# Performance work log

Measured on AMD Instinct MI355X. Metric: run time of the kernel, lower is better.

Reference implementation:

```python
import jax, jax.numpy as jnp
import numpy as np

N_HEAD = 16
HEAD_DIM = 64


def setup_inputs() -> dict:
    key = jax.random.key(0)
    k1, k2, k3 = jax.random.split(key, 3)
    B, T, C = 1, 4096, 1024
    x = jax.random.normal(k1, (B, T, C), dtype=jnp.float32)
    w_attn = jax.random.normal(k2, (3 * C, C), dtype=jnp.float32) * (C ** -0.5)
    w_proj = jax.random.normal(k3, (C, C), dtype=jnp.float32) * (C ** -0.5)
    return {"x": x, "w_attn": w_attn, "w_proj": w_proj}


def reference(x, w_attn, w_proj):
    B, T, C = x.shape
    H, D = N_HEAD, HEAD_DIM
    qkv = jnp.einsum('btc,fc->btf', x, w_attn)  # [B,T,3C]
    q, k, v = jnp.split(qkv, 3, axis=-1)
    # [B,H,T,D]
    q = q.reshape(B, T, H, D).transpose(0, 2, 1, 3)
    k = k.reshape(B, T, H, D).transpose(0, 2, 1, 3)
    v = v.reshape(B, T, H, D).transpose(0, 2, 1, 3)
    scale = 1.0 / (D ** 0.5)
    att = jnp.einsum('bhqd,bhkd->bhqk', q, k) * scale  # [B,H,T,T]
    causal = jnp.tril(jnp.ones((T, T), dtype=bool))
    att = jnp.where(causal[None, None], att, -jnp.inf)
    att = jax.nn.softmax(att, axis=-1)
    y = jnp.einsum('bhqk,bhkd->bhqd', att, v)  # [B,H,T,D]
    y = y.transpose(0, 2, 1, 3).reshape(B, T, C)
    return jnp.einsum('btc,oc->bto', y, w_proj)
```

## Files before the change

kernel.cpp:

```cpp
#include <hip/hip_runtime.h>

typedef unsigned short u16;
typedef __bf16 bf16x8 __attribute__((ext_vector_type(8)));
typedef float f32x4 __attribute__((ext_vector_type(4)));

__device__ __forceinline__ u16 f2bf(float f) {
  union { float f; unsigned u; } v; v.f = f;
  return (u16)((v.u + 0x7fffu + ((v.u >> 16) & 1u)) >> 16);
}
__device__ __forceinline__ float bf2f(u16 h) {
  union { unsigned u; float f; } v; v.u = ((unsigned)h) << 16;
  return v.f;
}

__device__ __forceinline__ unsigned pkbf(float lo, float hi) {
  union { float f; unsigned u; } a, b; a.f = lo; b.f = hi;
  return __builtin_amdgcn_perm(b.u + 0x8000u, a.u + 0x8000u, 0x07060302u);
}

__device__ __forceinline__ float fexp2(float x) {
#if __has_builtin(__builtin_amdgcn_exp2f)
  return __builtin_amdgcn_exp2f(x);
#else
  return exp2f(x);
#endif
}

__device__ __forceinline__ void gld16(const u16* g, u16* l) {
  __builtin_amdgcn_global_load_lds(
      (const __attribute__((address_space(1))) void*)g,
      (__attribute__((address_space(3))) void*)l, 16, 0, 0);
}


__global__ __launch_bounds__(256) void cvt3(
    const float* __restrict__ x, const float* __restrict__ wa,
    const float* __restrict__ wp, u16* __restrict__ xb,
    u16* __restrict__ wab, u16* __restrict__ wpb)
{
  int b = blockIdx.x;
  const float* in; u16* out; int i;
  if (b < 2048)      { in = x;  out = xb;  i = b * 256 + threadIdx.x; }
  else if (b < 3584) { in = wa; out = wab; i = (b - 2048) * 256 + threadIdx.x; }
  else               { in = wp; out = wpb; i = (b - 3584) * 256 + threadIdx.x; }
  const float* p = in + (size_t)i * 8;
  float4 a = *(const float4*)p, c = *(const float4*)(p + 4);
  uint4 o;
  o.x = pkbf(a.x, a.y); o.y = pkbf(a.z, a.w);
  o.z = pkbf(c.x, c.y); o.w = pkbf(c.z, c.w);
  *(uint4*)&out[(size_t)i * 8] = o;
}

__global__ __launch_bounds__(256) void combine2(
    const u16* __restrict__ O0, const u16* __restrict__ O1,
    const float* __restrict__ l0, const float* __restrict__ l1,
    u16* __restrict__ y)
{
  int i = blockIdx.x * 256 + threadIdx.x;
  int e0 = i * 8;
  int row = e0 >> 10, h = (e0 & 1023) >> 6;
  float inv = 1.0f / (l0[row * 16 + h] + l1[row * 16 + h]);
  uint4 a = *(const uint4*)&O0[(size_t)e0];
  uint4 b = *(const uint4*)&O1[(size_t)e0];
  unsigned aw[4] = {a.x, a.y, a.z, a.w}, bw[4] = {b.x, b.y, b.z, b.w};
  uint4 o;
  unsigned ow[4];
#pragma unroll
  for (int j = 0; j < 4; ++j) {
    float lo = (bf2f((u16)(aw[j] & 0xffffu)) + bf2f((u16)(bw[j] & 0xffffu))) * inv;
    float hi = (bf2f((u16)(aw[j] >> 16))     + bf2f((u16)(bw[j] >> 16)))     * inv;
    ow[j] = pkbf(lo, hi);
  }
  o.x = ow[0]; o.y = ow[1]; o.z = ow[2]; o.w = ow[3];
  *(uint4*)&y[(size_t)e0] = o;
}

template<bool COUT_F32, bool VSPLIT>
__global__ __launch_bounds__(256, 3) void gemm_lds(
    const u16* __restrict__ A, const u16* __restrict__ B, void* __restrict__ C,
    u16* __restrict__ C2, int M, int N, int K, int ldc)
{
  __shared__ u16 S[9216];
  u16* As = S;
  u16* Bs = S + 4096;
  const int tid  = threadIdx.x;
  const int wave = tid >> 6, lane = tid & 63;
  const int quad = lane >> 4, ln = lane & 15;
  const int m0 = blockIdx.y * 128, n0 = blockIdx.x * 128;
  const int wm = (wave >> 1) * 64, wn = (wave & 1) * 64;

  const int srow = wave * 32 + (lane >> 2);
  const int scol = (lane & 3) * 8;

  f32x4 acc[4][4] = {};

  for (int k0 = 0; k0 < K; k0 += 32) {
    __syncthreads();
    const u16* ga = A + (size_t)(m0 + srow) * K + k0 + scol;
    const u16* gb = B + (size_t)(n0 + srow) * K + k0 + scol;
    gld16(ga,                  As + wave * 1024);
    gld16(ga + (size_t)16 * K, As + wave * 1024 + 512);
    gld16(gb,                  Bs + wave * 1024);
    gld16(gb + (size_t)16 * K, Bs + wave * 1024 + 512);
    __syncthreads();

    bf16x8 af[4], bfr[4];
#pragma unroll
    for (int i = 0; i < 4; ++i) af[i]  = *(const bf16x8*)&As[(wm + i * 16 + ln) * 32 + quad * 8];
#pragma unroll
    for (int j = 0; j < 4; ++j) bfr[j] = *(const bf16x8*)&Bs[(wn + j * 16 + ln) * 32 + quad * 8];
#pragma unroll
    for (int i = 0; i < 4; ++i)
#pragma unroll
      for (int j = 0; j < 4; ++j)
        acc[i][j] = __builtin_amdgcn_mfma_f32_16x16x32_bf16(af[i], bfr[j], acc[i][j], 0, 0, 0);
  }

  if constexpr (VSPLIT) {
    if (n0 >= 2048) {
      u16 (*Cs)[72] = (u16(*)[72])S;
      __syncthreads();
#pragma unroll
      for (int c = 0; c < 2; ++c) {
        if ((wave >> 1) == c) {
#pragma unroll
          for (int i = 0; i < 4; ++i)
#pragma unroll
            for (int j = 0; j < 4; ++j)
#pragma unroll
              for (int r = 0; r < 4; ++r) {
                int pos = (i >> 1) * 32 + quad * 8 + (i & 1) * 4 + r;
                Cs[wn + j * 16 + ln][pos] = f2bf(acc[i][j][r]);
              }
        }
        __syncthreads();
        {
          int nl = tid >> 1, mseg = (tid & 1) * 32;
#pragma unroll
          for (int s2 = 0; s2 < 4; ++s2) {
            uint4 v4 = *(const uint4*)&Cs[nl][mseg + s2 * 8];
            *(uint4*)&C2[(size_t)(n0 - 2048 + nl) * 4096 + m0 + c * 64 + mseg + s2 * 8] = v4;
          }
        }
        __syncthreads();
      }
      return;
    }
  }

#pragma unroll
  for (int i = 0; i < 4; ++i)
#pragma unroll
    for (int j = 0; j < 4; ++j)
#pragma unroll
      for (int r = 0; r < 4; ++r) {
        int m = m0 + wm + i * 16 + quad * 4 + r;
        int n = n0 + wn + j * 16 + ln;
        if constexpr (COUT_F32)
          ((float*)C)[(size_t)m * ldc + n] = acc[i][j][r];
        else
          ((u16*)C)[(size_t)m * ldc + n] = f2bf(acc[i][j][r]);
      }
}

template<bool COUT_F32>
__global__ __launch_bounds__(256, 4) void gemm_mn(
    const u16* __restrict__ A, const u16* __restrict__ B, void* __restrict__ C,
    int M, int N, int K, int ldc)
{
  __shared__ u16 S[6144];
  u16* As = S;
  u16* Bs = S + 4096;
  const int tid  = threadIdx.x;
  const int wave = tid >> 6, lane = tid & 63;
  const int quad = lane >> 4, ln = lane & 15;
  const int m0 = blockIdx.y * 128, n0 = blockIdx.x * 64;
  const int wm = (wave >> 1) * 64, wn = (wave & 1) * 32;

  const int srow  = wave * 32 + (lane >> 2);
  const int srowB = wave * 16 + (lane >> 2);
  const int scol  = (lane & 3) * 8;

  f32x4 acc[4][2] = {};

  for (int k0 = 0; k0 < K; k0 += 32) {
    __syncthreads();
    const u16* ga = A + (size_t)(m0 + srow) * K + k0 + scol;
    gld16(ga,                  As + wave * 1024);
    gld16(ga + (size_t)16 * K, As + wave * 1024 + 512);
    gld16(B + (size_t)(n0 + srowB) * K + k0 + scol, Bs + wave * 512);
    __syncthreads();

    bf16x8 af[4], bfr[2];
#pragma unroll
    for (int i = 0; i < 4; ++i) af[i]  = *(const bf16x8*)&As[(wm + i * 16 + ln) * 32 + quad * 8];
#pragma unroll
    for (int j = 0; j < 2; ++j) bfr[j] = *(const bf16x8*)&Bs[(wn + j * 16 + ln) * 32 + quad * 8];
#pragma unroll
    for (int i = 0; i < 4; ++i)
#pragma unroll
      for (int j = 0; j < 2; ++j)
        acc[i][j] = __builtin_amdgcn_mfma_f32_16x16x32_bf16(af[i], bfr[j], acc[i][j], 0, 0, 0);
  }

#pragma unroll
  for (int i = 0; i < 4; ++i)
#pragma unroll
    for (int j = 0; j < 2; ++j)
#pragma unroll
      for (int r = 0; r < 4; ++r) {
        int m = m0 + wm + i * 16 + quad * 4 + r;
        int n = n0 + wn + j * 16 + ln;
        if constexpr (COUT_F32)
          ((float*)C)[(size_t)m * ldc + n] = acc[i][j][r];
        else
          ((u16*)C)[(size_t)m * ldc + n] = f2bf(acc[i][j][r]);
      }
}

template<bool F32>
__device__ __forceinline__ void stage8(u16* dst, const void* base, size_t off) {
  if constexpr (F32) {
    const float* p = (const float*)base + off;
    float4 a = *(const float4*)p;
    float4 b = *(const float4*)(p + 4);
    uint4 q;
    q.x = pkbf(a.x, a.y); q.y = pkbf(a.z, a.w);
    q.z = pkbf(b.x, b.y); q.w = pkbf(b.z, b.w);
    *(uint4*)dst = q;
  } else {
    *(uint4*)dst = *(const uint4*)((const u16*)base + off);
  }
}

template<bool AF32, bool BF32, bool COUT_F32, bool VSPLIT>
__global__ __launch_bounds__(256) void gemm_bt(
    const void* __restrict__ A, const void* __restrict__ B, void* __restrict__ C,
    u16* __restrict__ C2, int M, int N, int K, int ldc)
{
  __shared__ u16 As[128][40];
  __shared__ u16 Bs[128][40];
  const int tid  = threadIdx.x;
  const int wave = tid >> 6, lane = tid & 63;
  const int quad = lane >> 4, ln = lane & 15;
  const int m0 = blockIdx.y * 128, n0 = blockIdx.x * 128;
  const int wm = (wave >> 1) * 64, wn = (wave & 1) * 64;

  f32x4 acc[4][4] = {};

  for (int k0 = 0; k0 < K; k0 += 32) {
    __syncthreads();
#pragma unroll
    for (int i = 0; i < 2; ++i) {
      int idx = tid + i * 256;
      int row = idx >> 2, seg = (idx & 3) * 8;
      stage8<AF32>(&As[row][seg], A, (size_t)(m0 + row) * K + k0 + seg);
      stage8<BF32>(&Bs[row][seg], B, (size_t)(n0 + row) * K + k0 + seg);
    }
    __syncthreads();
    bf16x8 af[4], bfr[4];
#pragma unroll
    for (int i = 0; i < 4; ++i) af[i]  = *(const bf16x8*)&As[wm + i * 16 + ln][quad * 8];
#pragma unroll
    for (int j = 0; j < 4; ++j) bfr[j] = *(const bf16x8*)&Bs[wn + j * 16 + ln][quad * 8];
#pragma unroll
    for (int i = 0; i < 4; ++i)
#pragma unroll
      for (int j = 0; j < 4; ++j)
        acc[i][j] = __builtin_amdgcn_mfma_f32_16x16x32_bf16(af[i], bfr[j], acc[i][j], 0, 0, 0);
  }

  if constexpr (VSPLIT) {
    if (n0 >= 2048) {
      __shared__ u16 Cs[128][72];
#pragma unroll
      for (int c = 0; c < 2; ++c) {
        if ((wave >> 1) == c) {
#pragma unroll
          for (int i = 0; i < 4; ++i)
#pragma unroll
            for (int j = 0; j < 4; ++j)
#pragma unroll
              for (int r = 0; r < 4; ++r) {
                int pos = (i >> 1) * 32 + quad * 8 + (i & 1) * 4 + r;
                Cs[wn + j * 16 + ln][pos] = f2bf(acc[i][j][r]);
              }
        }
        __syncthreads();
        {
          int nl = tid >> 1, mseg = (tid & 1) * 32;
#pragma unroll
          for (int s2 = 0; s2 < 4; ++s2) {
            uint4 v4 = *(const uint4*)&Cs[nl][mseg + s2 * 8];
            *(uint4*)&C2[(size_t)(n0 - 2048 + nl) * 4096 + m0 + c * 64 + mseg + s2 * 8] = v4;
          }
        }
        __syncthreads();
      }
      return;
    }
  }

#pragma unroll
  for (int i = 0; i < 4; ++i)
#pragma unroll
    for (int j = 0; j < 4; ++j)
#pragma unroll
      for (int r = 0; r < 4; ++r) {
        int m = m0 + wm + i * 16 + quad * 4 + r;
        int n = n0 + wn + j * 16 + ln;
        if constexpr (COUT_F32)
          ((float*)C)[(size_t)m * ldc + n] = acc[i][j][r];
        else
          ((u16*)C)[(size_t)m * ldc + n] = f2bf(acc[i][j][r]);
      }
}

struct StageRegs { uint4 k0, k1, v0, v1; };

__device__ __forceinline__ StageRegs attn_stage_load(
    const u16* __restrict__ qk, const u16* __restrict__ vT,
    int h, int kbase, int tid) {
  StageRegs s;
  {
    int key = tid >> 2, seg = (tid & 3) * 16;
    const u16* kp = qk + (size_t)(kbase + key) * 2048 + 1024 + h * 64 + seg;
    s.k0 = *(const uint4*)kp;
    s.k1 = *(const uint4*)(kp + 8);
  }
  {
    int kh = tid >> 7, d = (tid >> 1) & 63, sg = (tid & 1) * 16;
    const u16* vp = vT + (size_t)(h * 64 + d) * 4096 + kbase + kh * 32 + sg;
    s.v0 = *(const uint4*)vp;
    s.v1 = *(const uint4*)(vp + 8);
  }
  return s;
}

template<bool SPLIT>
__global__ __launch_bounds__(256, SPLIT ? 3 : 2) void attn_fwd(
    const u16* __restrict__ qk, const u16* __restrict__ vT,
    u16* __restrict__ out0, u16* __restrict__ out1,
    float* __restrict__ l0buf, float* __restrict__ l1buf)
{
  __shared__ __align__(16) u16 Ks[2][8][65][8];
  __shared__ __align__(16) u16 Vt[2][8][65][8];

  const int tid  = threadIdx.x;
  const int wave = tid >> 6, lane = tid & 63;
  const int quad = lane >> 4, ln = lane & 15;
  const int bx = blockIdx.x;
  int qt, h, ktb, kte;
  u16* oout; float* lout;
  if constexpr (SPLIT) {
    qt = 31 - (bx >> 5);
    int half = (bx >> 4) & 1;
    h = bx & 15;
    ktb = half ? (qt + 1) : 0;
    kte = half ? (2 * qt + 1) : qt;
    oout = half ? out1 : out0;
    lout = half ? l1buf : l0buf;
  } else {
    qt = (bx < 256) ? (31 - (bx >> 4)) : ((bx - 256) >> 4);
    h = bx & 15;
    ktb = 0; kte = 2 * qt + 1;
    oout = out0; lout = nullptr;
  }
  const float C1 = 0.18033688f;

  const int sq0[2] = { qt * 128 + wave * 32, qt * 128 + wave * 32 + 16 };

  bf16x8 qa[2][2];
#pragma unroll
  for (int s = 0; s < 2; ++s) {
    const u16* qrow = qk + (size_t)(sq0[s] + ln) * 2048 + h * 64;
    qa[s][0] = *(const bf16x8*)(qrow + quad * 8);
    qa[s][1] = *(const bf16x8*)(qrow + 32 + quad * 8);
  }

  bf16x8 ones;
#pragma unroll
  for (int i = 0; i < 8; ++i) ones[i] = (__bf16)1.0f;

  f32x4 o[2][4] = {};
  f32x4 la[2] = {};

  StageRegs st = attn_stage_load(qk, vT, h, ktb * 64, tid);
  int b = 0;
  for (int kt = ktb; kt <= kte; ++kt, b ^= 1) {
    {
      int key = tid >> 2, seg = (tid & 3) * 16;
      int hf = seg >> 5, q0 = (seg & 31) >> 3;
      *(uint4*)&Ks[b][hf * 4 + q0][key][0]     = st.k0;
      *(uint4*)&Ks[b][hf * 4 + q0 + 1][key][0] = st.k1;
      int vh = tid >> 7, d = (tid >> 1) & 63, sq = (tid & 1) * 2;
      *(uint4*)&Vt[b][vh * 4 + sq][d][0]     = st.v0;
      *(uint4*)&Vt[b][vh * 4 + sq + 1][d][0] = st.v1;
    }
    __syncthreads();
    if (kt < kte) st = attn_stage_load(qk, vT, h, (kt + 1) * 64, tid);

    bool act[2];
#pragma unroll
    for (int s = 0; s < 2; ++s) act[s] = (kt * 64 <= sq0[s] + 15);

#pragma unroll 1
    for (int s2 = 0; s2 < 2; ++s2) {
      bf16x8 kf[2][2], vb[4];
#pragma unroll
      for (int hf = 0; hf < 2; ++hf)
#pragma unroll
        for (int tp = 0; tp < 2; ++tp)
          kf[hf][tp] = *(const bf16x8*)&Ks[b][hf * 4 + quad][(s2 * 2 + tp) * 16 + ln][0];
#pragma unroll
      for (int dt = 0; dt < 4; ++dt)
        vb[dt] = *(const bf16x8*)&Vt[b][s2 * 4 + quad][dt * 16 + ln][0];

#pragma unroll
      for (int s = 0; s < 2; ++s) {
        if (!act[s]) continue;
        f32x4 sv[2];
#pragma unroll
        for (int tp = 0; tp < 2; ++tp) {
          f32x4 z = {0.f, 0.f, 0.f, 0.f};
          z = __builtin_amdgcn_mfma_f32_16x16x32_bf16(kf[0][tp], qa[s][0], z, 0, 0, 0);
          z = __builtin_amdgcn_mfma_f32_16x16x32_bf16(kf[1][tp], qa[s][1], z, 0, 0, 0);
          sv[tp] = z;
        }
        float p[2][4];
        if (kt * 64 + 63 > sq0[s]) {
          const int qr = sq0[s] + ln;
#pragma unroll
          for (int tp = 0; tp < 2; ++tp) {
            int keyb = kt * 64 + (s2 * 2 + tp) * 16 + quad * 4;
#pragma unroll
            for (int r = 0; r < 4; ++r) {
              float arg = (keyb + r > qr) ? -200.0f : fmaf(sv[tp][r], C1, -46.0f);
              p[tp][r] = fexp2(arg);
            }
          }
        } else {
#pragma unroll
          for (int tp = 0; tp < 2; ++tp)
#pragma unroll
            for (int r = 0; r < 4; ++r)
              p[tp][r] = fexp2(fmaf(sv[tp][r], C1, -46.0f));
        }
        bf16x8 pv;
        pv[0] = (__bf16)p[0][0]; pv[1] = (__bf16)p[0][1];
        pv[2] = (__bf16)p[0][2]; pv[3] = (__bf16)p[0][3];
        pv[4] = (__bf16)p[1][0]; pv[5] = (__bf16)p[1][1];
        pv[6] = (__bf16)p[1][2]; pv[7] = (__bf16)p[1][3];
        la[s] = __builtin_amdgcn_mfma_f32_16x16x32_bf16(ones, pv, la[s], 0, 0, 0);
#pragma unroll
        for (int dt = 0; dt < 4; ++dt)
          o[s][dt] = __builtin_amdgcn_mfma_f32_16x16x32_bf16(vb[dt], pv, o[s][dt], 0, 0, 0);
      }
    }
  }

#pragma unroll
  for (int s = 0; s < 2; ++s) {
    int rowg = sq0[s] + ln;
    float l_s = la[s][0];
    if constexpr (SPLIT) {
#pragma unroll
      for (int dt = 0; dt < 4; ++dt) {
        uint2 w;
        w.x = pkbf(o[s][dt][0], o[s][dt][1]);
        w.y = pkbf(o[s][dt][2], o[s][dt][3]);
        *(uint2*)&oout[(size_t)rowg * 1024 + h * 64 + dt * 16 + quad * 4] = w;
      }
      if (quad == 0) lout[rowg * 16 + h] = l_s;
    } else {
      float inv = 1.0f / l_s;
#pragma unroll
      for (int dt = 0; dt < 4; ++dt) {
        uint2 w;
        w.x = pkbf(o[s][dt][0] * inv, o[s][dt][1] * inv);
        w.y = pkbf(o[s][dt][2] * inv, o[s][dt][3] * inv);
        *(uint2*)&oout[(size_t)rowg * 1024 + h * 64 + dt * 16 + quad * 4] = w;
      }
    }
  }
}

extern "C" void kernel_launch(void* const* d_in, const int* in_sizes, int n_in,
                              void* d_out, int out_size, void* d_ws, size_t ws_size,
                              hipStream_t stream) {
  const float* x      = (const float*)d_in[0];
  const float* w_attn = (const float*)d_in[1];
  const float* w_proj = (const float*)d_in[2];

  char* ws = (char*)d_ws;
  u16* qk = (u16*)ws;
  u16* vT = (u16*)(ws + (16u << 20));

  if (ws_size >= (size_t)(44u << 20)) {
    u16*   wpb = (u16*)(ws + (24u << 20));
    u16*   xb  = (u16*)(ws + (26u << 20));
    u16*   wab = (u16*)(ws + (34u << 20));
    u16*   Op0 = (u16*)(ws + (26u << 20));
    u16*   Op1 = (u16*)(ws + (34u << 20));
    float* l0  = (float*)(ws + (42u << 20));
    float* l1  = (float*)(ws + (42u << 20) + (256u << 10));
    u16*   y   = (u16*)ws;

    cvt3<<<4096, 256, 0, stream>>>(x, w_attn, w_proj, xb, wab, wpb);
    gemm_lds<false, true><<<dim3(24, 32), 256, 0, stream>>>(
        xb, wab, qk, vT, 4096, 3072, 1024, 2048);
    attn_fwd<true><<<dim3(1024), 256, 0, stream>>>(qk, vT, Op0, Op1, l0, l1);
    combine2<<<2048, 256, 0, stream>>>(Op0, Op1, l0, l1, y);
    gemm_mn<true><<<dim3(16, 32), 256, 0, stream>>>(
        y, wpb, d_out, 4096, 1024, 1024, 1024);
  } else if (ws_size >= (size_t)(40u << 20)) {
    u16* wpb = (u16*)(ws + (24u << 20));
    u16* xb  = (u16*)(ws + (26u << 20));
    u16* wab = (u16*)(ws + (34u << 20));
    u16* y   = (u16*)(ws + (26u << 20));

    cvt3<<<4096, 256, 0, stream>>>(x, w_attn, w_proj, xb, wab, wpb);
    gemm_lds<false, true><<<dim3(24, 32), 256, 0, stream>>>(
        xb, wab, qk, vT, 4096, 3072, 1024, 2048);
    attn_fwd<false><<<dim3(512), 256, 0, stream>>>(qk, vT, y, nullptr, nullptr, nullptr);
    gemm_mn<true><<<dim3(16, 32), 256, 0, stream>>>(
        y, wpb, d_out, 4096, 1024, 1024, 1024);
  } else {
    u16* y = (u16*)(ws + (24u << 20));
    gemm_bt<true, true, false, true><<<dim3(24, 32), 256, 0, stream>>>(
        x, w_attn, qk, vT, 4096, 3072, 1024, 2048);
    attn_fwd<false><<<dim3(512), 256, 0, stream>>>(qk, vT, y, nullptr, nullptr, nullptr);
    gemm_bt<false, true, true, false><<<dim3(8, 32), 256, 0, stream>>>(
        y, w_proj, d_out, nullptr, 4096, 1024, 1024, 1024);
  }
}
```

Baseline: 185.8 us.

## Use persistent attention blocks with atomic work-queue scheduling

The split attention kernel becomes persistent: 768 blocks (3 per CU on 256 CUs) take work items from a global atomic counter until all 1024 tiles are done. The counter is reset inside the conversion kernel. Items are handed out from the largest query tiles first, so load should balance dynamically across CUs instead of depending on hardware block dispatch order. The cost is two extra barriers and an atomic per tile, plus reliance on the counter being reset before each launch.

```diff
diff --git a/kernel.cpp b/kernel.cpp
--- a/kernel.cpp
+++ b/kernel.cpp
@@ -36,9 +36,10 @@
 __global__ __launch_bounds__(256) void cvt3(
     const float* __restrict__ x, const float* __restrict__ wa,
     const float* __restrict__ wp, u16* __restrict__ xb,
-    u16* __restrict__ wab, u16* __restrict__ wpb)
+    u16* __restrict__ wab, u16* __restrict__ wpb, int* __restrict__ ctr)
 {
   int b = blockIdx.x;
+  if (ctr && b == 0 && threadIdx.x == 0) *ctr = 0;
   const float* in; u16* out; int i;
   if (b < 2048)      { in = x;  out = xb;  i = b * 256 + threadIdx.x; }
   else if (b < 3584) { in = wa; out = wab; i = (b - 2048) * 256 + threadIdx.x; }
@@ -341,147 +342,164 @@
 __global__ __launch_bounds__(256, SPLIT ? 3 : 2) void attn_fwd(
     const u16* __restrict__ qk, const u16* __restrict__ vT,
     u16* __restrict__ out0, u16* __restrict__ out1,
-    float* __restrict__ l0buf, float* __restrict__ l1buf)
+    float* __restrict__ l0buf, float* __restrict__ l1buf,
+    int* __restrict__ ctr)
 {
   __shared__ __align__(16) u16 Ks[2][8][65][8];
   __shared__ __align__(16) u16 Vt[2][8][65][8];
+  __shared__ int jshare;
 
   const int tid  = threadIdx.x;
   const int wave = tid >> 6, lane = tid & 63;
   const int quad = lane >> 4, ln = lane & 15;
-  const int bx = blockIdx.x;
-  int qt, h, ktb, kte;
-  u16* oout; float* lout;
-  if constexpr (SPLIT) {
-    qt = 31 - (bx >> 5);
-    int half = (bx >> 4) & 1;
-    h = bx & 15;
-    ktb = half ? (qt + 1) : 0;
-    kte = half ? (2 * qt + 1) : qt;
-    oout = half ? out1 : out0;
-    lout = half ? l1buf : l0buf;
-  } else {
-    qt = (bx < 256) ? (31 - (bx >> 4)) : ((bx - 256) >> 4);
-    h = bx & 15;
-    ktb = 0; kte = 2 * qt + 1;
-    oout = out0; lout = nullptr;
-  }
   const float C1 = 0.18033688f;
 
-  const int sq0[2] = { qt * 128 + wave * 32, qt * 128 + wave * 32 + 16 };
-
-  bf16x8 qa[2][2];
-#pragma unroll
-  for (int s = 0; s < 2; ++s) {
-    const u16* qrow = qk + (size_t)(sq0[s] + ln) * 2048 + h * 64;
-    qa[s][0] = *(const bf16x8*)(qrow + quad * 8);
-    qa[s][1] = *(const bf16x8*)(qrow + 32 + quad * 8);
-  }
-
   bf16x8 ones;
 #pragma unroll
   for (int i = 0; i < 8; ++i) ones[i] = (__bf16)1.0f;
 
-  f32x4 o[2][4] = {};
-  f32x4 la[2] = {};
-
-  StageRegs st = attn_stage_load(qk, vT, h, ktb * 64, tid);
-  int b = 0;
-  for (int kt = ktb; kt <= kte; ++kt, b ^= 1) {
-    {
-      int key = tid >> 2, seg = (tid & 3) * 16;
-      int hf = seg >> 5, q0 = (seg & 31) >> 3;
-      *(uint4*)&Ks[b][hf * 4 + q0][key][0]     = st.k0;
-      *(uint4*)&Ks[b][hf * 4 + q0 + 1][key][0] = st.k1;
-      int vh = tid >> 7, d = (tid >> 1) & 63, sq = (tid & 1) * 2;
-      *(uint4*)&Vt[b][vh * 4 + sq][d][0]     = st.v0;
-      *(uint4*)&Vt[b][vh * 4 + sq + 1][d][0] = st.v1;
-    }
-    __syncthreads();
-    if (kt < kte) st = attn_stage_load(qk, vT, h, (kt + 1) * 64, tid);
-
-    bool act[2];
-#pragma unroll
-    for (int s = 0; s < 2; ++s) act[s] = (kt * 64 <= sq0[s] + 15);
+  for (;;) {
+    int j;
+    if constexpr (SPLIT) {
+      __syncthreads();
+      if (tid == 0) jshare = atomicAdd(ctr, 1);
+      __syncthreads();
+      j = jshare;
+      if (j >= 1024) break;
+    } else {
+      j = blockIdx.x;
+    }
+
+    int qt, h, ktb, kte;
+    u16* oout; float* lout;
+    if constexpr (SPLIT) {
+      qt = 31 - (j >> 5);
+      int half = (j >> 4) & 1;
+      h = j & 15;
+      ktb = half ? (qt + 1) : 0;
+      kte = half ? (2 * qt + 1) : qt;
+      oout = half ? out1 : out0;
+      lout = half ? l1buf : l0buf;
+    } else {
+      qt = (j < 256) ? (31 - (j >> 4)) : ((j - 256) >> 4);
+      h = j & 15;
+      ktb = 0; kte = 2 * qt + 1;
+      oout = out0; lout = nullptr;
+    }
+
+    const int sq0[2] = { qt * 128 + wave * 32, qt * 128 + wave * 32 + 16 };
+
+    bf16x8 qa[2][2];
+#pragma unroll
+    for (int s = 0; s < 2; ++s) {
+      const u16* qrow = qk + (size_t)(sq0[s] + ln) * 2048 + h * 64;
+      qa[s][0] = *(const bf16x8*)(qrow + quad * 8);
+      qa[s][1] = *(const bf16x8*)(qrow + 32 + quad * 8);
+    }
+
+    f32x4 o[2][4] = {};
+    f32x4 la[2] = {};
+
+    StageRegs st = attn_stage_load(qk, vT, h, ktb * 64, tid);
+    int b = 0;
+    for (int kt = ktb; kt <= kte; ++kt, b ^= 1) {
+      {
+        int key = tid >> 2, seg = (tid & 3) * 16;
+        int hf = seg >> 5, q0 = (seg & 31) >> 3;
+        *(uint4*)&Ks[b][hf * 4 + q0][key][0]     = st.k0;
+        *(uint4*)&Ks[b][hf * 4 + q0 + 1][key][0] = st.k1;
+        int vh = tid >> 7, d = (tid >> 1) & 63, sq = (tid & 1) * 2;
+        *(uint4*)&Vt[b][vh * 4 + sq][d][0]     = st.v0;
+        *(uint4*)&Vt[b][vh * 4 + sq + 1][d][0] = st.v1;
+      }
+      __syncthreads();
+      if (kt < kte) st = attn_stage_load(qk, vT, h, (kt + 1) * 64, tid);
+
+      bool act[2];
+#pragma unroll
+      for (int s = 0; s < 2; ++s) act[s] = (kt * 64 <= sq0[s] + 15);
 
 #pragma unroll 1
-    for (int s2 = 0; s2 < 2; ++s2) {
-      bf16x8 kf[2][2], vb[4];
-#pragma unroll
-      for (int hf = 0; hf < 2; ++hf)
-#pragma unroll
-        for (int tp = 0; tp < 2; ++tp)
-          kf[hf][tp] = *(const bf16x8*)&Ks[b][hf * 4 + quad][(s2 * 2 + tp) * 16 + ln][0];
-#pragma unroll
-      for (int dt = 0; dt < 4; ++dt)
-        vb[dt] = *(const bf16x8*)&Vt[b][s2 * 4 + quad][dt * 16 + ln][0];
-
-#pragma unroll
-      for (int s = 0; s < 2; ++s) {
-        if (!act[s]) continue;
-        f32x4 sv[2];
-#pragma unroll
-        for (int tp = 0; tp < 2; ++tp) {
-          f32x4 z = {0.f, 0.f, 0.f, 0.f};
-          z = __builtin_amdgcn_mfma_f32_16x16x32_bf16(kf[0][tp], qa[s][0], z, 0, 0, 0);
-          z = __builtin_amdgcn_mfma_f32_16x16x32_bf16(kf[1][tp], qa[s][1], z, 0, 0, 0);
-          sv[tp] = z;
-        }
-        float p[2][4];
-        if (kt * 64 + 63 > sq0[s]) {
-          const int qr = sq0[s] + ln;
+      for (int s2 = 0; s2 < 2; ++s2) {
+        bf16x8 kf[2][2], vb[4];
+#pragma unroll
+        for (int hf = 0; hf < 2; ++hf)
+#pragma unroll
+          for (int tp = 0; tp < 2; ++tp)
+            kf[hf][tp] = *(const bf16x8*)&Ks[b][hf * 4 + quad][(s2 * 2 + tp) * 16 + ln][0];
+#pragma unroll
+        for (int dt = 0; dt < 4; ++dt)
+          vb[dt] = *(const bf16x8*)&Vt[b][s2 * 4 + quad][dt * 16 + ln][0];
+
+#pragma unroll
+        for (int s = 0; s < 2; ++s) {
+          if (!act[s]) continue;
+          f32x4 sv[2];
 #pragma unroll
           for (int tp = 0; tp < 2; ++tp) {
-            int keyb = kt * 64 + (s2 * 2 + tp) * 16 + quad * 4;
-#pragma unroll
-            for (int r = 0; r < 4; ++r) {
-              float arg = (keyb + r > qr) ? -200.0f : fmaf(sv[tp][r], C1, -46.0f);
-              p[tp][r] = fexp2(arg);
+            f32x4 z = {0.f, 0.f, 0.f, 0.f};
+            z = __builtin_amdgcn_mfma_f32_16x16x32_bf16(kf[0][tp], qa[s][0], z, 0, 0, 0);
+            z = __builtin_amdgcn_mfma_f32_16x16x32_bf16(kf[1][tp], qa[s][1], z, 0, 0, 0);
+            sv[tp] = z;
+          }
+          float p[2][4];
+          if (kt * 64 + 63 > sq0[s]) {
+            const int qr = sq0[s] + ln;
+#pragma unroll
+            for (int tp = 0; tp < 2; ++tp) {
+              int keyb = kt * 64 + (s2 * 2 + tp) * 16 + quad * 4;
+#pragma unroll
+              for (int r = 0; r < 4; ++r) {
+                float arg = (keyb + r > qr) ? -200.0f : fmaf(sv[tp][r], C1, -46.0f);
+                p[tp][r] = fexp2(arg);
+              }
             }
+          } else {
+#pragma unroll
+            for (int tp = 0; tp < 2; ++tp)
+#pragma unroll
+              for (int r = 0; r < 4; ++r)
+                p[tp][r] = fexp2(fmaf(sv[tp][r], C1, -46.0f));
           }
-        } else {
-#pragma unroll
-          for (int tp = 0; tp < 2; ++tp)
-#pragma unroll
-            for (int r = 0; r < 4; ++r)
-              p[tp][r] = fexp2(fmaf(sv[tp][r], C1, -46.0f));
-        }
-        bf16x8 pv;
-        pv[0] = (__bf16)p[0][0]; pv[1] = (__bf16)p[0][1];
-        pv[2] = (__bf16)p[0][2]; pv[3] = (__bf16)p[0][3];
-        pv[4] = (__bf16)p[1][0]; pv[5] = (__bf16)p[1][1];
-        pv[6] = (__bf16)p[1][2]; pv[7] = (__bf16)p[1][3];
-        la[s] = __builtin_amdgcn_mfma_f32_16x16x32_bf16(ones, pv, la[s], 0, 0, 0);
-#pragma unroll
-        for (int dt = 0; dt < 4; ++dt)
-          o[s][dt] = __builtin_amdgcn_mfma_f32_16x16x32_bf16(vb[dt], pv, o[s][dt], 0, 0, 0);
-      }
-    }
-  }
-
-#pragma unroll
-  for (int s = 0; s < 2; ++s) {
-    int rowg = sq0[s] + ln;
-    float l_s = la[s][0];
-    if constexpr (SPLIT) {
-#pragma unroll
-      for (int dt = 0; dt < 4; ++dt) {
-        uint2 w;
-        w.x = pkbf(o[s][dt][0], o[s][dt][1]);
-        w.y = pkbf(o[s][dt][2], o[s][dt][3]);
-        *(uint2*)&oout[(size_t)rowg * 1024 + h * 64 + dt * 16 + quad * 4] = w;
-      }
-      if (quad == 0) lout[rowg * 16 + h] = l_s;
-    } else {
-      float inv = 1.0f / l_s;
-#pragma unroll
-      for (int dt = 0; dt < 4; ++dt) {
-        uint2 w;
-        w.x = pkbf(o[s][dt][0] * inv, o[s][dt][1] * inv);
-        w.y = pkbf(o[s][dt][2] * inv, o[s][dt][3] * inv);
-        *(uint2*)&oout[(size_t)rowg * 1024 + h * 64 + dt * 16 + quad * 4] = w;
-      }
-    }
+          bf16x8 pv;
+          pv[0] = (__bf16)p[0][0]; pv[1] = (__bf16)p[0][1];
+          pv[2] = (__bf16)p[0][2]; pv[3] = (__bf16)p[0][3];
+          pv[4] = (__bf16)p[1][0]; pv[5] = (__bf16)p[1][1];
+          pv[6] = (__bf16)p[1][2]; pv[7] = (__bf16)p[1][3];
+          la[s] = __builtin_amdgcn_mfma_f32_16x16x32_bf16(ones, pv, la[s], 0, 0, 0);
+#pragma unroll
+          for (int dt = 0; dt < 4; ++dt)
+            o[s][dt] = __builtin_amdgcn_mfma_f32_16x16x32_bf16(vb[dt], pv, o[s][dt], 0, 0, 0);
+        }
+      }
+    }
+
+#pragma unroll
+    for (int s = 0; s < 2; ++s) {
+      int rowg = sq0[s] + ln;
+      float l_s = la[s][0];
+      if constexpr (SPLIT) {
+#pragma unroll
+        for (int dt = 0; dt < 4; ++dt) {
+          uint2 w;
+          w.x = pkbf(o[s][dt][0], o[s][dt][1]);
+          w.y = pkbf(o[s][dt][2], o[s][dt][3]);
+          *(uint2*)&oout[(size_t)rowg * 1024 + h * 64 + dt * 16 + quad * 4] = w;
+        }
+        if (quad == 0) lout[rowg * 16 + h] = l_s;
+      } else {
+        float inv = 1.0f / l_s;
+#pragma unroll
+        for (int dt = 0; dt < 4; ++dt) {
+          uint2 w;
+          w.x = pkbf(o[s][dt][0] * inv, o[s][dt][1] * inv);
+          w.y = pkbf(o[s][dt][2] * inv, o[s][dt][3] * inv);
+          *(uint2*)&oout[(size_t)rowg * 1024 + h * 64 + dt * 16 + quad * 4] = w;
+        }
+      }
+    }
+
+    if constexpr (!SPLIT) break;
   }
 }
 
@@ -504,12 +522,13 @@
     u16*   Op1 = (u16*)(ws + (34u << 20));
     float* l0  = (float*)(ws + (42u << 20));
     float* l1  = (float*)(ws + (42u << 20) + (256u << 10));
+    int*   ctr = (int*)(ws + (42u << 20) + (512u << 10));
     u16*   y   = (u16*)ws;
 
-    cvt3<<<4096, 256, 0, stream>>>(x, w_attn, w_proj, xb, wab, wpb);
+    cvt3<<<4096, 256, 0, stream>>>(x, w_attn, w_proj, xb, wab, wpb, ctr);
     gemm_lds<false, true><<<dim3(24, 32), 256, 0, stream>>>(
         xb, wab, qk, vT, 4096, 3072, 1024, 2048);
-    attn_fwd<true><<<dim3(1024), 256, 0, stream>>>(qk, vT, Op0, Op1, l0, l1);
+    attn_fwd<true><<<dim3(768), 256, 0, stream>>>(qk, vT, Op0, Op1, l0, l1, ctr);
     combine2<<<2048, 256, 0, stream>>>(Op0, Op1, l0, l1, y);
     gemm_mn<true><<<dim3(16, 32), 256, 0, stream>>>(
         y, wpb, d_out, 4096, 1024, 1024, 1024);
@@ -519,17 +538,17 @@
     u16* wab = (u16*)(ws + (34u << 20));
     u16* y   = (u16*)(ws + (26u << 20));
 
-    cvt3<<<4096, 256, 0, stream>>>(x, w_attn, w_proj, xb, wab, wpb);
+    cvt3<<<4096, 256, 0, stream>>>(x, w_attn, w_proj, xb, wab, wpb, nullptr);
     gemm_lds<false, true><<<dim3(24, 32), 256, 0, stream>>>(
         xb, wab, qk, vT, 4096, 3072, 1024, 2048);
-    attn_fwd<false><<<dim3(512), 256, 0, stream>>>(qk, vT, y, nullptr, nullptr, nullptr);
+    attn_fwd<false><<<dim3(512), 256, 0, stream>>>(qk, vT, y, nullptr, nullptr, nullptr, nullptr);
     gemm_mn<true><<<dim3(16, 32), 256, 0, stream>>>(
         y, wpb, d_out, 4096, 1024, 1024, 1024);
   } else {
     u16* y = (u16*)(ws + (24u << 20));
     gemm_bt<true, true, false, true><<<dim3(24, 32), 256, 0, stream>>>(
         x, w_attn, qk, vT, 4096, 3072, 1024, 2048);
-    attn_fwd<false><<<dim3(512), 256, 0, stream>>>(qk, vT, y, nullptr, nullptr, nullptr);
+    attn_fwd<false><<<dim3(512), 256, 0, stream>>>(qk, vT, y, nullptr, nullptr, nullptr, nullptr);
     gemm_bt<false, true, true, false><<<dim3(8, 32), 256, 0, stream>>>(
         y, w_proj, d_out, nullptr, 4096, 1024, 1024, 1024);
   }
```

After: 204.4 us. 1.1x slower.

## Double GEMM K-step to 64 and add XCD-aware workgroup swizzle

Applied to the files above, without the earlier changes.

Both projection GEMM kernels now stage two 32-wide K slices per iteration into separate LDS buffers, which halves the number of barrier pairs per K and lets more loads be in flight. Block indices are also remapped so that consecutive flat workgroup IDs, which are spread across the chiplets, map to contiguous tiles on each chiplet for better L2 reuse. The cost is doubled LDS per block, which may reduce occupancy. The swizzle also assumes the grid size divides evenly by 8.

```diff
diff --git a/kernel.cpp b/kernel.cpp
--- a/kernel.cpp
+++ b/kernel.cpp
@@ -80,13 +80,20 @@
     const u16* __restrict__ A, const u16* __restrict__ B, void* __restrict__ C,
     u16* __restrict__ C2, int M, int N, int K, int ldc)
 {
-  __shared__ u16 S[9216];
-  u16* As = S;
-  u16* Bs = S + 4096;
+  __shared__ u16 S[16384];
+  u16* As0 = S;
+  u16* As1 = S + 4096;
+  u16* Bs0 = S + 8192;
+  u16* Bs1 = S + 12288;
   const int tid  = threadIdx.x;
   const int wave = tid >> 6, lane = tid & 63;
   const int quad = lane >> 4, ln = lane & 15;
-  const int m0 = blockIdx.y * 128, n0 = blockIdx.x * 128;
+
+  int nwgx = gridDim.x;
+  int flat = blockIdx.y * nwgx + blockIdx.x;
+  int cpx  = (nwgx * gridDim.y) >> 3;
+  int swz  = (flat & 7) * cpx + (flat >> 3);
+  const int m0 = (swz / nwgx) * 128, n0 = (swz % nwgx) * 128;
   const int wm = (wave >> 1) * 64, wn = (wave & 1) * 64;
 
   const int srow = wave * 32 + (lane >> 2);
@@ -94,21 +101,34 @@
 
   f32x4 acc[4][4] = {};
 
-  for (int k0 = 0; k0 < K; k0 += 32) {
+  for (int k0 = 0; k0 < K; k0 += 64) {
     __syncthreads();
     const u16* ga = A + (size_t)(m0 + srow) * K + k0 + scol;
     const u16* gb = B + (size_t)(n0 + srow) * K + k0 + scol;
-    gld16(ga,                  As + wave * 1024);
-    gld16(ga + (size_t)16 * K, As + wave * 1024 + 512);
-    gld16(gb,                  Bs + wave * 1024);
-    gld16(gb + (size_t)16 * K, Bs + wave * 1024 + 512);
+    gld16(ga,                       As0 + wave * 1024);
+    gld16(ga + (size_t)16 * K,      As0 + wave * 1024 + 512);
+    gld16(ga + 32,                  As1 + wave * 1024);
+    gld16(ga + (size_t)16 * K + 32, As1 + wave * 1024 + 512);
+    gld16(gb,                       Bs0 + wave * 1024);
+    gld16(gb + (size_t)16 * K,      Bs0 + wave * 1024 + 512);
+    gld16(gb + 32,                  Bs1 + wave * 1024);
+    gld16(gb + (size_t)16 * K + 32, Bs1 + wave * 1024 + 512);
     __syncthreads();
 
     bf16x8 af[4], bfr[4];
 #pragma unroll
-    for (int i = 0; i < 4; ++i) af[i]  = *(const bf16x8*)&As[(wm + i * 16 + ln) * 32 + quad * 8];
-#pragma unroll
-    for (int j = 0; j < 4; ++j) bfr[j] = *(const bf16x8*)&Bs[(wn + j * 16 + ln) * 32 + quad * 8];
+    for (int i = 0; i < 4; ++i) af[i]  = *(const bf16x8*)&As0[(wm + i * 16 + ln) * 32 + quad * 8];
+#pragma unroll
+    for (int j = 0; j < 4; ++j) bfr[j] = *(const bf16x8*)&Bs0[(wn + j * 16 + ln) * 32 + quad * 8];
+#pragma unroll
+    for (int i = 0; i < 4; ++i)
+#pragma unroll
+      for (int j = 0; j < 4; ++j)
+        acc[i][j] = __builtin_amdgcn_mfma_f32_16x16x32_bf16(af[i], bfr[j], acc[i][j], 0, 0, 0);
+#pragma unroll
+    for (int i = 0; i < 4; ++i) af[i]  = *(const bf16x8*)&As1[(wm + i * 16 + ln) * 32 + quad * 8];
+#pragma unroll
+    for (int j = 0; j < 4; ++j) bfr[j] = *(const bf16x8*)&Bs1[(wn + j * 16 + ln) * 32 + quad * 8];
 #pragma unroll
     for (int i = 0; i < 4; ++i)
 #pragma unroll
@@ -168,13 +188,20 @@
     const u16* __restrict__ A, const u16* __restrict__ B, void* __restrict__ C,
     int M, int N, int K, int ldc)
 {
-  __shared__ u16 S[6144];
-  u16* As = S;
-  u16* Bs = S + 4096;
+  __shared__ u16 S[12288];
+  u16* As0 = S;
+  u16* As1 = S + 4096;
+  u16* Bs0 = S + 8192;
+  u16* Bs1 = S + 10240;
   const int tid  = threadIdx.x;
   const int wave = tid >> 6, lane = tid & 63;
   const int quad = lane >> 4, ln = lane & 15;
-  const int m0 = blockIdx.y * 128, n0 = blockIdx.x * 64;
+
+  int nwgx = gridDim.x;
+  int flat = blockIdx.y * nwgx + blockIdx.x;
+  int cpx  = (nwgx * gridDim.y) >> 3;
+  int swz  = (flat & 7) * cpx + (flat >> 3);
+  const int m0 = (swz / nwgx) * 128, n0 = (swz % nwgx) * 64;
   const int wm = (wave >> 1) * 64, wn = (wave & 1) * 32;
 
   const int srow  = wave * 32 + (lane >> 2);
@@ -183,19 +210,32 @@
 
   f32x4 acc[4][2] = {};
 
-  for (int k0 = 0; k0 < K; k0 += 32) {
+  for (int k0 = 0; k0 < K; k0 += 64) {
     __syncthreads();
     const u16* ga = A + (size_t)(m0 + srow) * K + k0 + scol;
-    gld16(ga,                  As + wave * 1024);
-    gld16(ga + (size_t)16 * K, As + wave * 1024 + 512);
-    gld16(B + (size_t)(n0 + srowB) * K + k0 + scol, Bs + wave * 512);
+    const u16* gb = B + (size_t)(n0 + srowB) * K + k0 + scol;
+    gld16(ga,                       As0 + wave * 1024);
+    gld16(ga + (size_t)16 * K,      As0 + wave * 1024 + 512);
+    gld16(ga + 32,                  As1 + wave * 1024);
+    gld16(ga + (size_t)16 * K + 32, As1 + wave * 1024 + 512);
+    gld16(gb,                       Bs0 + wave * 512);
+    gld16(gb + 32,                  Bs1 + wave * 512);
     __syncthreads();
 
     bf16x8 af[4], bfr[2];
 #pragma unroll
-    for (int i = 0; i < 4; ++i) af[i]  = *(const bf16x8*)&As[(wm + i * 16 + ln) * 32 + quad * 8];
-#pragma unroll
-    for (int j = 0; j < 2; ++j) bfr[j] = *(const bf16x8*)&Bs[(wn + j * 16 + ln) * 32 + quad * 8];
+    for (int i = 0; i < 4; ++i) af[i]  = *(const bf16x8*)&As0[(wm + i * 16 + ln) * 32 + quad * 8];
+#pragma unroll
+    for (int j = 0; j < 2; ++j) bfr[j] = *(const bf16x8*)&Bs0[(wn + j * 16 + ln) * 32 + quad * 8];
+#pragma unroll
+    for (int i = 0; i < 4; ++i)
+#pragma unroll
+      for (int j = 0; j < 2; ++j)
+        acc[i][j] = __builtin_amdgcn_mfma_f32_16x16x32_bf16(af[i], bfr[j], acc[i][j], 0, 0, 0);
+#pragma unroll
+    for (int i = 0; i < 4; ++i) af[i]  = *(const bf16x8*)&As1[(wm + i * 16 + ln) * 32 + quad * 8];
+#pragma unroll
+    for (int j = 0; j < 2; ++j) bfr[j] = *(const bf16x8*)&Bs1[(wn + j * 16 + ln) * 32 + quad * 8];
 #pragma unroll
     for (int i = 0; i < 4; ++i)
 #pragma unroll
```

Result: no change. 187.7 us (+1.0%).

## Fuse split-attention combine into output projection GEMM A-operand staging

Applied to the files above, without the earlier changes.

Removes the separate combine2 kernel and instead merges the two partial attention outputs, normalizes them by the summed denominators, and packs to bf16 while staging the A tile of the output projection GEMM. The intent is to drop one kernel launch and the write and reread of the intermediate y buffer. In exchange each GEMM block redoes the combine arithmetic for its A rows, once per N-tile column (16 times), and issues more global loads per k-step. It also switches to a hardware reciprocal, and the GEMM uses a 128x64 tile with register prefetch of the next A tile.

```diff
diff --git a/kernel.cpp b/kernel.cpp
--- a/kernel.cpp
+++ b/kernel.cpp
@@ -23,6 +23,14 @@
   return __builtin_amdgcn_exp2f(x);
 #else
   return exp2f(x);
+#endif
+}
+
+__device__ __forceinline__ float frcp(float x) {
+#if __has_builtin(__builtin_amdgcn_rcpf)
+  return __builtin_amdgcn_rcpf(x);
+#else
+  return 1.0f / x;
 #endif
 }
 
@@ -51,29 +59,6 @@
   *(uint4*)&out[(size_t)i * 8] = o;
 }
 
-__global__ __launch_bounds__(256) void combine2(
-    const u16* __restrict__ O0, const u16* __restrict__ O1,
-    const float* __restrict__ l0, const float* __restrict__ l1,
-    u16* __restrict__ y)
-{
-  int i = blockIdx.x * 256 + threadIdx.x;
-  int e0 = i * 8;
-  int row = e0 >> 10, h = (e0 & 1023) >> 6;
-  float inv = 1.0f / (l0[row * 16 + h] + l1[row * 16 + h]);
-  uint4 a = *(const uint4*)&O0[(size_t)e0];
-  uint4 b = *(const uint4*)&O1[(size_t)e0];
-  unsigned aw[4] = {a.x, a.y, a.z, a.w}, bw[4] = {b.x, b.y, b.z, b.w};
-  uint4 o;
-  unsigned ow[4];
-#pragma unroll
-  for (int j = 0; j < 4; ++j) {
-    float lo = (bf2f((u16)(aw[j] & 0xffffu)) + bf2f((u16)(bw[j] & 0xffffu))) * inv;
-    float hi = (bf2f((u16)(aw[j] >> 16))     + bf2f((u16)(bw[j] >> 16)))     * inv;
-    ow[j] = pkbf(lo, hi);
-  }
-  o.x = ow[0]; o.y = ow[1]; o.z = ow[2]; o.w = ow[3];
-  *(uint4*)&y[(size_t)e0] = o;
-}
 
 template<bool COUT_F32, bool VSPLIT>
 __global__ __launch_bounds__(256, 3) void gemm_lds(
@@ -212,9 +197,94 @@
         int m = m0 + wm + i * 16 + quad * 4 + r;
         int n = n0 + wn + j * 16 + ln;
         if constexpr (COUT_F32)
-          ((float*)C)[(size_t)m * ldc + n] = acc[i][j][r];
+          ((float*)C)[(size_t)m * ldc + n] = acc[j == 0 ? i : i][j][r];
         else
           ((u16*)C)[(size_t)m * ldc + n] = f2bf(acc[i][j][r]);
+      }
+}
+
+struct CmbRegs { uint4 a0, b0, a1, b1; float inv0, inv1; };
+
+__device__ __forceinline__ CmbRegs cmb_load(
+    const u16* __restrict__ O0, const u16* __restrict__ O1,
+    const float* __restrict__ l0, const float* __restrict__ l1,
+    int r0, int c) {
+  CmbRegs v;
+  size_t e0 = (size_t)r0 * 1024 + c;
+  size_t e1 = e0 + (size_t)16 * 1024;
+  v.a0 = *(const uint4*)&O0[e0]; v.b0 = *(const uint4*)&O1[e0];
+  v.a1 = *(const uint4*)&O0[e1]; v.b1 = *(const uint4*)&O1[e1];
+  int h = c >> 6;
+  v.inv0 = frcp(l0[r0 * 16 + h]        + l1[r0 * 16 + h]);
+  v.inv1 = frcp(l0[(r0 + 16) * 16 + h] + l1[(r0 + 16) * 16 + h]);
+  return v;
+}
+
+__device__ __forceinline__ uint4 cmb_pack(uint4 a, uint4 b, float inv) {
+  unsigned aw[4] = {a.x, a.y, a.z, a.w}, bw[4] = {b.x, b.y, b.z, b.w};
+  unsigned ow[4];
+#pragma unroll
+  for (int j = 0; j < 4; ++j) {
+    float lo = (bf2f((u16)(aw[j] & 0xffffu)) + bf2f((u16)(bw[j] & 0xffffu))) * inv;
+    float hi = (bf2f((u16)(aw[j] >> 16))     + bf2f((u16)(bw[j] >> 16)))     * inv;
+    ow[j] = pkbf(lo, hi);
+  }
+  uint4 o; o.x = ow[0]; o.y = ow[1]; o.z = ow[2]; o.w = ow[3];
+  return o;
+}
+
+__global__ __launch_bounds__(256, 4) void gemm_mn_cmb(
+    const u16* __restrict__ O0, const u16* __restrict__ O1,
+    const float* __restrict__ l0, const float* __restrict__ l1,
+    const u16* __restrict__ B, float* __restrict__ C,
+    int K, int ldc)
+{
+  __shared__ u16 S[6144];
+  u16* As = S;
+  u16* Bs = S + 4096;
+  const int tid  = threadIdx.x;
+  const int wave = tid >> 6, lane = tid & 63;
+  const int quad = lane >> 4, ln = lane & 15;
+  const int m0 = blockIdx.y * 128, n0 = blockIdx.x * 64;
+  const int wm = (wave >> 1) * 64, wn = (wave & 1) * 32;
+
+  const int srow  = wave * 32 + (lane >> 2);
+  const int srowB = wave * 16 + (lane >> 2);
+  const int scol  = (lane & 3) * 8;
+
+  f32x4 acc[4][2] = {};
+
+  CmbRegs ld = cmb_load(O0, O1, l0, l1, m0 + srow, scol);
+  for (int k0 = 0; k0 < K; k0 += 32) {
+    __syncthreads();
+    gld16(B + (size_t)(n0 + srowB) * K + k0 + scol, Bs + wave * 512);
+    *(uint4*)&As[srow * 32 + scol]        = cmb_pack(ld.a0, ld.b0, ld.inv0);
+    *(uint4*)&As[(srow + 16) * 32 + scol] = cmb_pack(ld.a1, ld.b1, ld.inv1);
+    __syncthreads();
+    if (k0 + 32 < K)
+      ld = cmb_load(O0, O1, l0, l1, m0 + srow, k0 + 32 + scol);
+
+    bf16x8 af[4], bfr[2];
+#pragma unroll
+    for (int i = 0; i < 4; ++i) af[i]  = *(const bf16x8*)&As[(wm + i * 16 + ln) * 32 + quad * 8];
+#pragma unroll
+    for (int j = 0; j < 2; ++j) bfr[j] = *(const bf16x8*)&Bs[(wn + j * 16 + ln) * 32 + quad * 8];
+#pragma unroll
+    for (int i = 0; i < 4; ++i)
+#pragma unroll
+      for (int j = 0; j < 2; ++j)
+        acc[i][j] = __builtin_amdgcn_mfma_f32_16x16x32_bf16(af[i], bfr[j], acc[i][j], 0, 0, 0);
+  }
+
+#pragma unroll
+  for (int i = 0; i < 4; ++i)
+#pragma unroll
+    for (int j = 0; j < 2; ++j)
+#pragma unroll
+      for (int r = 0; r < 4; ++r) {
+        int m = m0 + wm + i * 16 + quad * 4 + r;
+        int n = n0 + wn + j * 16 + ln;
+        C[(size_t)m * ldc + n] = acc[i][j][r];
       }
 }
 
@@ -504,15 +574,13 @@
     u16*   Op1 = (u16*)(ws + (34u << 20));
     float* l0  = (float*)(ws + (42u << 20));
     float* l1  = (float*)(ws + (42u << 20) + (256u << 10));
-    u16*   y   = (u16*)ws;
 
     cvt3<<<4096, 256, 0, stream>>>(x, w_attn, w_proj, xb, wab, wpb);
     gemm_lds<false, true><<<dim3(24, 32), 256, 0, stream>>>(
         xb, wab, qk, vT, 4096, 3072, 1024, 2048);
     attn_fwd<true><<<dim3(1024), 256, 0, stream>>>(qk, vT, Op0, Op1, l0, l1);
-    combine2<<<2048, 256, 0, stream>>>(Op0, Op1, l0, l1, y);
-    gemm_mn<true><<<dim3(16, 32), 256, 0, stream>>>(
-        y, wpb, d_out, 4096, 1024, 1024, 1024);
+    gemm_mn_cmb<<<dim3(16, 32), 256, 0, stream>>>(
+        Op0, Op1, l0, l1, wpb, (float*)d_out, 1024, 1024);
   } else if (ws_size >= (size_t)(40u << 20)) {
     u16* wpb = (u16*)(ws + (24u << 20));
     u16* xb  = (u16*)(ws + (26u << 20));
```

New measurement: 200.2 us. 1.08x slower.
